# Optimization experiments

Measured on AMD Instinct MI355X. Metric: run time of the kernel, lower is better.

The kernel has to match this reference:

```python
import jax, jax.numpy as jnp
import numpy as np

N = 50000
E = 400000  # bidirectional: second half is reverse of first half
D = 128
T = 3
EPS = 1e-09


def apply_lambda(x, log_dt, log_lambda_real, lambda_imag, one_minus=False):
    # lambda_complex = exp((-exp(log_lambda_real) + 1j*lambda_imag) * dt)
    dt = jnp.exp(log_dt)
    mag = jnp.exp(-jnp.exp(log_lambda_real) * dt)          # |lambda| [D//2]
    mag = jnp.where(one_minus, 1.0 - mag, mag)
    phase = lambda_imag * dt                                # angle (cos/sin are wrap-invariant)
    c, s = jnp.cos(phase), jnp.sin(phase)
    xp = x.reshape(x.shape[:-1] + (-1, 2))                  # [..., D//2, 2]
    xr = (c * xp[..., 0] - s * xp[..., 1]) * mag
    xi = (s * xp[..., 0] + c * xp[..., 1]) * mag
    return jnp.stack((xr, xi), axis=-1).reshape(x.shape)


def setup_inputs() -> dict:
    key = jax.random.key(0)
    kx, ke1, ke2, k1, k2, k3, k4 = jax.random.split(key, 7)
    x = jax.random.normal(kx, (N, D), dtype=jnp.float32)
    a = jax.random.randint(ke1, (E // 2,), 0, N)
    b = jax.random.randint(ke2, (E // 2,), 0, N)
    edge_index = jnp.stack([jnp.concatenate([a, b]), jnp.concatenate([b, a])], axis=0)
    hidden = D + D
    scale1 = 1.0 / np.sqrt(D)
    scale2 = 1.0 / np.sqrt(hidden)
    return {
        "x": x,
        "edge_index": edge_index,
        "log_dt": jnp.asarray(np.log(0.1), dtype=jnp.float32),
        "log_lambda_real": jnp.full((D // 2,), np.log(0.5), dtype=jnp.float32),
        "lambda_imag": jnp.arange(D // 2, dtype=jnp.float32) * np.pi,
        "W1": jax.random.uniform(k1, (D, hidden), jnp.float32, -scale1, scale1),
        "W2": jax.random.uniform(k2, (D, hidden), jnp.float32, -scale1, scale1),
        "Wp": jax.random.uniform(k3, (hidden, D), jnp.float32, -scale2, scale2),
        "bp": jax.random.uniform(k4, (D,), jnp.float32, -scale2, scale2),
    }


def reference(x, edge_index, log_dt, log_lambda_real, lambda_imag, W1, W2, Wp, bp):
    x_in = x  # dim_in == dim_out -> residual from pre-MLP input
    # MLP: silu(x W1) * (x W2) -> proj
    h = jax.nn.silu(x @ W1) * (x @ W2)
    x = h @ Wp + bp

    lam = lambda v, om=False: apply_lambda(v, log_dt, log_lambda_real, lambda_imag, om)
    src, dst = edge_index[0], edge_index[1]

    deg = jax.ops.segment_sum(jnp.ones((E,), x.dtype), src, num_segments=N)  # [N]
    M = x[src]                                                              # [E, D]
    m = jax.ops.segment_sum(M, dst, num_segments=N)                         # [N, D]

    for _ in range(T):
        M_ji = jnp.concatenate((M[E // 2:], M[:E // 2]), axis=0)            # reverse-edge message
        x_e = x[src]
        deg_e = deg[src][:, None]
        M = jnp.where(deg_e == 1,
                      x_e,
                      lam(x_e, True) + lam(m[src] - M_ji) / (deg_e - 1 + EPS))
        m = jax.ops.segment_sum(M, dst, num_segments=N)

    out = jnp.where(deg[:, None] == 0, x, lam(x, True) + lam(m) / (deg[:, None] + EPS))
    out = jax.nn.relu(out)  # dropout p=0 (eval)
    return x_in + out
```

## Files before the change

kernel.cpp:

```cpp
#include <hip/hip_runtime.h>

#define EPSF 1e-9f

typedef __bf16 bf16x8 __attribute__((ext_vector_type(8)));
typedef float  f32x4  __attribute__((ext_vector_type(4)));
typedef unsigned short ushort_t;
typedef unsigned int uint_t;
typedef ushort_t us8 __attribute__((ext_vector_type(8)));

__device__ __forceinline__ float2 cmul(float cr, float ci, float2 v) {
    return make_float2(cr * v.x - ci * v.y, ci * v.x + cr * v.y);
}

__device__ __forceinline__ ushort_t f2bf(float f) {
    unsigned int u = __float_as_uint(f);
    u += 0x7FFFu + ((u >> 16) & 1u);
    return (ushort_t)(u >> 16);
}

__device__ __forceinline__ float2 bfu2(uint_t u) {
    return make_float2(__uint_as_float(u << 16), __uint_as_float(u & 0xFFFF0000u));
}
__device__ __forceinline__ uint_t packbf(float2 v) {
    return ((uint_t)f2bf(v.y) << 16) | (uint_t)f2bf(v.x);
}

__global__ void k_init(const float* __restrict__ ldt, const float* __restrict__ llr,
                       const float* __restrict__ lim, float* __restrict__ tab,
                       int* __restrict__ cnt, int N) {
    int i = blockIdx.x * blockDim.x + threadIdx.x;
    if (i < N) cnt[i] = 0;
    if (blockIdx.x == 0 && threadIdx.x < 64) {
        int p = threadIdx.x;
        float dt  = expf(ldt[0]);
        float mag = expf(-expf(llr[p]) * dt);
        float ph  = lim[p] * dt;
        float c = cosf(ph), s = sinf(ph);
        float m2 = mag * mag, m3 = m2 * mag;
        float c2 = c * c - s * s, s2 = 2.f * c * s;
        float c3 = c2 * c - s2 * s, s3 = s2 * c + c2 * s;
        tab[p]        = c * mag;          tab[64 + p]  = s * mag;
        tab[128 + p]  = c * (1.f - mag);  tab[192 + p] = s * (1.f - mag);
        tab[256 + p]  = c2 * m2;          tab[320 + p] = s2 * m2;
        tab[384 + p]  = c3 * m3;          tab[448 + p] = s3 * m3;
    }
}

__global__ void k_prepw3(const float* __restrict__ W1, const float* __restrict__ W2,
                         const float* __restrict__ Wp, ushort_t* __restrict__ wb1,
                         ushort_t* __restrict__ wb2, ushort_t* __restrict__ wpb) {
    int tid = blockIdx.x * blockDim.x + threadIdx.x;
    const float* w; ushort_t* wb; int ncols, nsteps;
    if (tid < 4096)       { w = W1; wb = wb1; ncols = 256; nsteps = 4; }
    else if (tid < 8192)  { tid -= 4096; w = W2; wb = wb2; ncols = 256; nsteps = 4; }
    else                  { tid -= 8192; w = Wp; wb = wpb; ncols = 128; nsteps = 8; }
    int l  = tid & 63;
    int s  = (tid >> 6) % nsteps;
    int nt = tid / (64 * nsteps);
    int col = nt * 16 + (l & 15);
    int kb  = s * 32 + (l >> 4) * 8;
    us8 d;
#pragma unroll
    for (int j = 0; j < 8; ++j) d[j] = f2bf(w[(size_t)(kb + j) * ncols + col]);
    *(us8*)(wb + (size_t)tid * 8) = d;
}

__global__ void __launch_bounds__(256)
k_mlpf(const float* __restrict__ x, const ushort_t* __restrict__ wb1,
       const ushort_t* __restrict__ wb2, const ushort_t* __restrict__ wpb,
       const float* __restrict__ bp, ushort_t* __restrict__ xpb, int Mt) {
    __shared__ ushort_t hs[2][4096];
    const int wid = threadIdx.x >> 6, l = threadIdx.x & 63;
    const int mt0 = blockIdx.x * 2;
    const bool has1 = (mt0 + 1) < Mt;
    const int llo = l & 15, lhi = l >> 4;

    bf16x8 af[2][4];
#pragma unroll
    for (int m = 0; m < 2; ++m) {
        int mt = (m == 1 && !has1) ? mt0 : (mt0 + m);
        const float* xr = x + (size_t)(mt * 16 + llo) * 128 + lhi * 8;
#pragma unroll
        for (int s = 0; s < 4; ++s) {
            float4 v0 = *(const float4*)(xr + s * 32);
            float4 v1 = *(const float4*)(xr + s * 32 + 4);
            us8 d;
            d[0] = f2bf(v0.x); d[1] = f2bf(v0.y); d[2] = f2bf(v0.z); d[3] = f2bf(v0.w);
            d[4] = f2bf(v1.x); d[5] = f2bf(v1.y); d[6] = f2bf(v1.z); d[7] = f2bf(v1.w);
            af[m][s] = *(bf16x8*)&d;
        }
    }

    const bf16x8* B1 = (const bf16x8*)wb1;
    const bf16x8* B2 = (const bf16x8*)wb2;
    const bf16x8* BP = (const bf16x8*)wpb;
    const f32x4 zero = {0.f, 0.f, 0.f, 0.f};

#pragma unroll
    for (int j = 0; j < 4; ++j) {
        int nt = wid * 4 + j;
        bf16x8 b1[4], b2[4];
#pragma unroll
        for (int s = 0; s < 4; ++s) {
            b1[s] = B1[(nt * 4 + s) * 64 + l];
            b2[s] = B2[(nt * 4 + s) * 64 + l];
        }
#pragma unroll
        for (int m = 0; m < 2; ++m) {
            f32x4 a1 = zero, a2 = zero;
#pragma unroll
            for (int s = 0; s < 4; ++s) {
                a1 = __builtin_amdgcn_mfma_f32_16x16x32_bf16(af[m][s], b1[s], a1, 0, 0, 0);
                a2 = __builtin_amdgcn_mfma_f32_16x16x32_bf16(af[m][s], b2[s], a2, 0, 0, 0);
            }
#pragma unroll
            for (int i = 0; i < 4; ++i) {
                float g = a1[i];
                float hv = (g / (1.f + __expf(-g))) * a2[i];
                int r = 4 * lhi + i;
                int byte = (r << 9) + ((nt * 16 + llo) << 1);
                byte ^= (r & 7) << 4;
                hs[m][byte >> 1] = f2bf(hv);
            }
        }
    }
    __syncthreads();

#pragma unroll
    for (int j = 0; j < 2; ++j) {
        int nt3 = wid * 2 + j;
        f32x4 acc0 = zero, acc1 = zero;
#pragma unroll
        for (int sg = 0; sg < 8; ++sg) {
            bf16x8 bw = BP[(nt3 * 8 + sg) * 64 + l];
            int byte = (llo << 9) + (sg << 6) + (lhi << 4);
            byte ^= (llo & 7) << 4;
            bf16x8 h0 = *(const bf16x8*)((const char*)hs[0] + byte);
            acc0 = __builtin_amdgcn_mfma_f32_16x16x32_bf16(h0, bw, acc0, 0, 0, 0);
            bf16x8 h1 = *(const bf16x8*)((const char*)hs[1] + byte);
            acc1 = __builtin_amdgcn_mfma_f32_16x16x32_bf16(h1, bw, acc1, 0, 0, 0);
        }
        float bpv = bp[nt3 * 16 + llo];
        {
            const int row0 = mt0 * 16;
#pragma unroll
            for (int i = 0; i < 4; ++i) {
                int r = row0 + 4 * lhi + i;
                xpb[(size_t)r * 128 + nt3 * 16 + llo] = f2bf(acc0[i] + bpv);
            }
        }
        if (has1) {
            const int row0 = (mt0 + 1) * 16;
#pragma unroll
            for (int i = 0; i < 4; ++i) {
                int r = row0 + 4 * lhi + i;
                xpb[(size_t)r * 128 + nt3 * 16 + llo] = f2bf(acc1[i] + bpv);
            }
        }
    }
}

__global__ void k_hist(const int* __restrict__ ei, int E, int* __restrict__ cnt) {
    int e = blockIdx.x * blockDim.x + threadIdx.x;
    if (e < E) atomicAdd(&cnt[ei[E + e]], 1);
}

__global__ void __launch_bounds__(256)
k_scanA(const int* __restrict__ cnt, int N, int* __restrict__ bsum) {
    __shared__ int s[256];
    int t = threadIdx.x;
    int i = blockIdx.x * 256 + t;
    int v = (i < N) ? cnt[i] : 0;
    s[t] = v;
    __syncthreads();
#pragma unroll
    for (int d = 128; d > 0; d >>= 1) {
        if (t < d) s[t] += s[t + d];
        __syncthreads();
    }
    if (t == 0) bsum[blockIdx.x] = s[0];
}

__global__ void __launch_bounds__(1024)
k_scanB(const int* __restrict__ bsum, int NB, int* __restrict__ bpre,
        int* __restrict__ offN) {
    __shared__ int s[1024];
    int t = threadIdx.x;
    int v = (t < NB) ? bsum[t] : 0;
    s[t] = v;
    __syncthreads();
    for (int d = 1; d < 1024; d <<= 1) {
        int u = (t >= d) ? s[t - d] : 0;
        __syncthreads();
        s[t] += u;
        __syncthreads();
    }
    if (t < NB) bpre[t] = s[t] - v;
    if (t == NB - 1) *offN = s[t];
}

__global__ void __launch_bounds__(256)
k_scanC(const int* __restrict__ cnt, int N, const int* __restrict__ bpre,
        int* __restrict__ off, int* __restrict__ cursor, float* __restrict__ bv) {
    __shared__ int s[256];
    int t = threadIdx.x;
    int i = blockIdx.x * 256 + t;
    int v = (i < N) ? cnt[i] : 0;
    s[t] = v;
    __syncthreads();
    for (int d = 1; d < 256; d <<= 1) {
        int u = (t >= d) ? s[t - d] : 0;
        __syncthreads();
        s[t] += u;
        __syncthreads();
    }
    if (i < N) {
        int excl = bpre[blockIdx.x] + s[t] - v;
        off[i] = excl;
        cursor[i] = excl;
        bv[i] = (v > 1) ? (-1.f / ((float)v - 1.f + EPSF)) : 0.f;
    }
}

__global__ void k_fill(const int* __restrict__ ei, int E, const float* __restrict__ bv,
                       int* __restrict__ cursor, uint2* __restrict__ csrb) {
    int e = blockIdx.x * blockDim.x + threadIdx.x;
    if (e < E) {
        int s = ei[e], d = ei[E + e];
        int p = atomicAdd(&cursor[d], 1);
        csrb[p] = make_uint2((uint_t)s, __float_as_uint(bv[s]));
    }
}

__global__ void __launch_bounds__(256)
k_passA(const ushort_t* __restrict__ xpb, const uint2* __restrict__ eb,
        const int* __restrict__ off, const float* __restrict__ tab,
        ushort_t* __restrict__ Xbb, ushort_t* __restrict__ a1b, int N) {
    int tid = blockIdx.x * blockDim.x + threadIdx.x;
    int v = tid >> 6, l = tid & 63;
    if (v >= N) return;
    int beg = off[v], end = off[v + 1];
    float2 m0 = make_float2(0.f, 0.f), xb = make_float2(0.f, 0.f);
    const uint_t* tb = (const uint_t*)xpb;
    int k = beg;
    for (; k + 7 < end; k += 8) {
        uint2 e[8];
#pragma unroll
        for (int j = 0; j < 8; ++j) e[j] = eb[k + j];
        uint_t u[8];
#pragma unroll
        for (int j = 0; j < 8; ++j) u[j] = tb[(size_t)e[j].x * 64 + l];
#pragma unroll
        for (int j = 0; j < 8; ++j) {
            float b = __uint_as_float(e[j].y);
            float2 t0 = bfu2(u[j]);
            m0.x += t0.x; m0.y += t0.y;
            xb.x += b * t0.x; xb.y += b * t0.y;
        }
    }
    for (; k < end; ++k) {
        uint2 e0 = eb[k];
        float2 t0 = bfu2(tb[(size_t)e0.x * 64 + l]);
        float b0 = __uint_as_float(e0.y);
        m0.x += t0.x; m0.y += t0.y;
        xb.x += b0 * t0.x; xb.y += b0 * t0.y;
    }
    ((uint_t*)Xbb)[(size_t)v * 64 + l] = packbf(xb);
    float2 xv = bfu2(tb[(size_t)v * 64 + l]);
    int dg = end - beg;
    float L1r = tab[l], L1i = tab[64 + l], O1r = tab[128 + l], O1i = tab[192 + l];
    float Q = 1.f / ((float)dg - 1.f + EPSF);
    float2 t1 = cmul(O1r, O1i, xv);
    float2 t2 = cmul(L1r, L1i, m0);
    float2 a = make_float2(t1.x + Q * t2.x, t1.y + Q * t2.y);
    if (dg == 1) a = xv;
    ((uint_t*)a1b)[(size_t)v * 64 + l] = packbf(a);
}

__global__ void __launch_bounds__(256)
k_passB(const ushort_t* __restrict__ xpb, const ushort_t* __restrict__ a1b,
        const uint2* __restrict__ eb, const int* __restrict__ off,
        const float* __restrict__ tab, ushort_t* __restrict__ ab1b,
        float* __restrict__ Bv, float* __restrict__ B2v,
        ushort_t* __restrict__ a2b, int N) {
    int tid = blockIdx.x * blockDim.x + threadIdx.x;
    int v = tid >> 6, l = tid & 63;
    if (v >= N) return;
    int beg = off[v], end = off[v + 1];
    float2 A1 = make_float2(0.f, 0.f), ab = make_float2(0.f, 0.f);
    float Bs = 0.f, B2s = 0.f;
    const uint_t* tb = (const uint_t*)a1b;
    int k = beg;
    for (; k + 7 < end; k += 8) {
        uint2 e[8];
#pragma unroll
        for (int j = 0; j < 8; ++j) e[j] = eb[k + j];
        uint_t u[8];
#pragma unroll
        for (int j = 0; j < 8; ++j) u[j] = tb[(size_t)e[j].x * 64 + l];
#pragma unroll
        for (int j = 0; j < 8; ++j) {
            float b = __uint_as_float(e[j].y);
            float2 t0 = bfu2(u[j]);
            A1.x += t0.x; A1.y += t0.y;
            ab.x += b * t0.x; ab.y += b * t0.y;
            Bs += b; B2s += b * b;
        }
    }
    for (; k < end; ++k) {
        uint2 e0 = eb[k];
        float2 t0 = bfu2(tb[(size_t)e0.x * 64 + l]);
        float b0 = __uint_as_float(e0.y);
        A1.x += t0.x; A1.y += t0.y;
        ab.x += b0 * t0.x; ab.y += b0 * t0.y;
        Bs += b0; B2s += b0 * b0;
    }
    ((uint_t*)ab1b)[(size_t)v * 64 + l] = packbf(ab);
    if (l == 0) { Bv[v] = Bs; B2v[v] = B2s; }
    float2 xv = bfu2(((const uint_t*)xpb)[(size_t)v * 64 + l]);
    int dg = end - beg;
    float L1r = tab[l], L1i = tab[64 + l], O1r = tab[128 + l], O1i = tab[192 + l];
    float2 lx = cmul(L1r, L1i, xv);
    float2 m1 = make_float2(A1.x + Bs * lx.x, A1.y + Bs * lx.y);
    float Q = 1.f / ((float)dg - 1.f + EPSF);
    float2 t1 = cmul(O1r, O1i, xv);
    float2 lm = cmul(L1r, L1i, m1);
    float2 a = make_float2(t1.x + Q * lm.x, t1.y + Q * lm.y);
    if (dg == 1) a = xv;
    ((uint_t*)a2b)[(size_t)v * 64 + l] = packbf(a);
}

__global__ void __launch_bounds__(256)
k_passC(const ushort_t* __restrict__ xpb, const ushort_t* __restrict__ a2b,
        const ushort_t* __restrict__ a1b, const ushort_t* __restrict__ Xbb,
        const float* __restrict__ bv, const float* __restrict__ Bv,
        const uint2* __restrict__ eb, const int* __restrict__ off,
        const float* __restrict__ tab, ushort_t* __restrict__ a3b, int N) {
    int tid = blockIdx.x * blockDim.x + threadIdx.x;
    int v = tid >> 6, l = tid & 63;
    if (v >= N) return;
    int beg = off[v], end = off[v + 1];
    float2 A2 = make_float2(0.f, 0.f);
    const uint_t* tb = (const uint_t*)a2b;
    int k = beg;
    for (; k + 7 < end; k += 8) {
        uint_t u[8];
#pragma unroll
        for (int j = 0; j < 8; ++j) u[j] = tb[(size_t)eb[k + j].x * 64 + l];
#pragma unroll
        for (int j = 0; j < 8; ++j) {
            float2 t0 = bfu2(u[j]);
            A2.x += t0.x; A2.y += t0.y;
        }
    }
    for (; k < end; ++k) {
        float2 t0 = bfu2(tb[(size_t)eb[k].x * 64 + l]);
        A2.x += t0.x; A2.y += t0.y;
    }
    float2 xv  = bfu2(((const uint_t*)xpb)[(size_t)v * 64 + l]);
    float2 a1v = bfu2(((const uint_t*)a1b)[(size_t)v * 64 + l]);
    float2 Xbv = bfu2(((const uint_t*)Xbb)[(size_t)v * 64 + l]);
    int dg = end - beg;
    float Bs = Bv[v], bs = bv[v];
    float L1r = tab[l], L1i = tab[64 + l], O1r = tab[128 + l], O1i = tab[192 + l];
    float L2r = tab[256 + l], L2i = tab[320 + l];
    float2 la1 = cmul(L1r, L1i, a1v);
    float2 lxb = cmul(L2r, L2i, Xbv);
    float2 m2 = make_float2(A2.x + Bs * la1.x + bs * lxb.x,
                            A2.y + Bs * la1.y + bs * lxb.y);
    float Q = 1.f / ((float)dg - 1.f + EPSF);
    float2 t1 = cmul(O1r, O1i, xv);
    float2 lm = cmul(L1r, L1i, m2);
    float2 a = make_float2(t1.x + Q * lm.x, t1.y + Q * lm.y);
    if (dg == 1) a = xv;
    ((uint_t*)a3b)[(size_t)v * 64 + l] = packbf(a);
}

__global__ void __launch_bounds__(256)
k_passD(const float* __restrict__ xin, const ushort_t* __restrict__ xpb,
        const ushort_t* __restrict__ a3b, const ushort_t* __restrict__ a2b,
        const ushort_t* __restrict__ ab1b, const float* __restrict__ bv,
        const float* __restrict__ Bv, const float* __restrict__ B2v,
        const uint2* __restrict__ eb, const int* __restrict__ off,
        const float* __restrict__ tab, float* __restrict__ out, int N) {
    int tid = blockIdx.x * blockDim.x + threadIdx.x;
    int v = tid >> 6, l = tid & 63;
    if (v >= N) return;
    int beg = off[v], end = off[v + 1];
    float2 A3 = make_float2(0.f, 0.f);
    const uint_t* tb = (const uint_t*)a3b;
    int k = beg;
    for (; k + 7 < end; k += 8) {
        uint_t u[8];
#pragma unroll
        for (int j = 0; j < 8; ++j) u[j] = tb[(size_t)eb[k + j].x * 64 + l];
#pragma unroll
        for (int j = 0; j < 8; ++j) {
            float2 t0 = bfu2(u[j]);
            A3.x += t0.x; A3.y += t0.y;
        }
    }
    for (; k < end; ++k) {
        float2 t0 = bfu2(tb[(size_t)eb[k].x * 64 + l]);
        A3.x += t0.x; A3.y += t0.y;
    }
    size_t o = (size_t)v * 128 + 2 * l;
    float2 xv  = bfu2(((const uint_t*)xpb)[(size_t)v * 64 + l]);
    float2 a2v = bfu2(((const uint_t*)a2b)[(size_t)v * 64 + l]);
    float2 Abv = bfu2(((const uint_t*)ab1b)[(size_t)v * 64 + l]);
    int dg = end - beg;
    float Bs = Bv[v], bs = bv[v], B2s = B2v[v];
    float L1r = tab[l], L1i = tab[64 + l], O1r = tab[128 + l], O1i = tab[192 + l];
    float L2r = tab[256 + l], L2i = tab[320 + l];
    float L3r = tab[384 + l], L3i = tab[448 + l];
    float2 la2 = cmul(L1r, L1i, a2v);
    float2 lab = cmul(L2r, L2i, Abv);
    float2 lx3 = cmul(L3r, L3i, xv);
    float bB2 = bs * B2s;
    float2 m3 = make_float2(A3.x + Bs * la2.x + bs * lab.x + bB2 * lx3.x,
                            A3.y + Bs * la2.y + bs * lab.y + bB2 * lx3.y);
    float2 g;
    if (dg == 0) {
        g = xv;
    } else {
        float inv = 1.f / ((float)dg + EPSF);
        float2 t1 = cmul(O1r, O1i, xv);
        float2 lm = cmul(L1r, L1i, m3);
        g = make_float2(t1.x + lm.x * inv, t1.y + lm.y * inv);
    }
    float2 xi = *(const float2*)&xin[o];
    float2 res = make_float2(xi.x + fmaxf(g.x, 0.f), xi.y + fmaxf(g.y, 0.f));
    *(float2*)&out[o] = res;
}

extern "C" void kernel_launch(void* const* d_in, const int* in_sizes, int n_in,
                              void* d_out, int out_size, void* d_ws, size_t ws_size,
                              hipStream_t stream) {
    const float* x   = (const float*)d_in[0];
    const int*   ei  = (const int*)d_in[1];
    const float* ldt = (const float*)d_in[2];
    const float* llr = (const float*)d_in[3];
    const float* lim = (const float*)d_in[4];
    const float* W1  = (const float*)d_in[5];
    const float* W2  = (const float*)d_in[6];
    const float* Wp  = (const float*)d_in[7];
    const float* bp  = (const float*)d_in[8];
    float* out = (float*)d_out;

    const int N = in_sizes[0] / 128;
    const int E = in_sizes[1] / 2;
    const size_t nd = (size_t)N * 128;
    const int Mt = (N + 15) / 16;
    const int Mt2 = (Mt + 1) / 2;
    const int NB = (N + 255) / 256;

    ushort_t* xpb  = (ushort_t*)d_ws;
    ushort_t* a1b  = xpb + nd;
    ushort_t* a2b  = a1b + nd;
    ushort_t* a3b  = a2b + nd;
    ushort_t* Xbb  = a3b + nd;
    ushort_t* ab1b = Xbb + nd;

    int*   cnt    = (int*)(ab1b + nd);
    int*   off    = cnt + N;
    int*   cursor = off + N + 4;
    float* bv     = (float*)(cursor + N);
    float* Bv     = bv + N;
    float* B2v    = Bv + N;
    float* tab    = B2v + N;
    int*   bsum   = (int*)(tab + 512);
    int*   bpre   = bsum + NB;
    uint2* csrb   = (uint2*)(bpre + NB + (NB & 1));
    ushort_t* wb1 = (ushort_t*)(csrb + E);
    ushort_t* wb2 = wb1 + 32768;
    ushort_t* wpb = wb2 + 32768;

    const int nodeBlocks = (int)(((size_t)N * 64 + 255) / 256);
    const int eBlocks    = (E + 255) / 256;

    k_init<<<NB, 256, 0, stream>>>(ldt, llr, lim, tab, cnt, N);

    k_prepw3<<<48, 256, 0, stream>>>(W1, W2, Wp, wb1, wb2, wpb);
    k_mlpf<<<Mt2, 256, 0, stream>>>(x, wb1, wb2, wpb, bp, xpb, Mt);

    k_hist<<<eBlocks, 256, 0, stream>>>(ei, E, cnt);
    k_scanA<<<NB, 256, 0, stream>>>(cnt, N, bsum);
    k_scanB<<<1, 1024, 0, stream>>>(bsum, NB, bpre, &off[N]);
    k_scanC<<<NB, 256, 0, stream>>>(cnt, N, bpre, off, cursor, bv);
    k_fill<<<eBlocks, 256, 0, stream>>>(ei, E, bv, cursor, csrb);

    k_passA<<<nodeBlocks, 256, 0, stream>>>(xpb, csrb, off, tab, Xbb, a1b, N);
    k_passB<<<nodeBlocks, 256, 0, stream>>>(xpb, a1b, csrb, off, tab, ab1b, Bv, B2v, a2b, N);
    k_passC<<<nodeBlocks, 256, 0, stream>>>(xpb, a2b, a1b, Xbb, bv, Bv, csrb, off, tab, a3b, N);
    k_passD<<<nodeBlocks, 256, 0, stream>>>(x, xpb, a3b, a2b, ab1b, bv, Bv, B2v, csrb, off, tab, out, N);
}
```

Measured before the change: 239.8 us.

## Pad CSR segments to multiples of eight with dummy zero-row edges

Each node's CSR segment is rounded up to a multiple of 8 entries and filled with dummy edges that point to an extra all-zero row at index N, appended to each gathered bf16 buffer. This lets every gather pass run only the unrolled 8-wide loop with no scalar tail, and the true degree now comes from cnt. The cost is an extra kernel that pre-fills the padded edge array, more gather traffic for the padding entries (mean degree is about 8), and extra workspace.

```diff
diff --git a/kernel.cpp b/kernel.cpp
--- a/kernel.cpp
+++ b/kernel.cpp
@@ -27,7 +27,9 @@
 
 __global__ void k_init(const float* __restrict__ ldt, const float* __restrict__ llr,
                        const float* __restrict__ lim, float* __restrict__ tab,
-                       int* __restrict__ cnt, int N) {
+                       int* __restrict__ cnt, int N,
+                       uint_t* __restrict__ xpbu, uint_t* __restrict__ a1bu,
+                       uint_t* __restrict__ a2bu, uint_t* __restrict__ a3bu) {
     int i = blockIdx.x * blockDim.x + threadIdx.x;
     if (i < N) cnt[i] = 0;
     if (blockIdx.x == 0 && threadIdx.x < 64) {
@@ -44,6 +46,10 @@
         tab[256 + p]  = c2 * m2;          tab[320 + p] = s2 * m2;
         tab[384 + p]  = c3 * m3;          tab[448 + p] = s3 * m3;
     }
+    if (blockIdx.x == 1 && threadIdx.x < 64) {
+        size_t o = (size_t)N * 64 + threadIdx.x;
+        xpbu[o] = 0u; a1bu[o] = 0u; a2bu[o] = 0u; a3bu[o] = 0u;
+    }
 }
 
 __global__ void k_prepw3(const float* __restrict__ W1, const float* __restrict__ W2,
@@ -170,7 +176,7 @@
     __shared__ int s[256];
     int t = threadIdx.x;
     int i = blockIdx.x * 256 + t;
-    int v = (i < N) ? cnt[i] : 0;
+    int v = (i < N) ? ((cnt[i] + 7) & ~7) : 0;
     s[t] = v;
     __syncthreads();
 #pragma unroll
@@ -205,7 +211,8 @@
     __shared__ int s[256];
     int t = threadIdx.x;
     int i = blockIdx.x * 256 + t;
-    int v = (i < N) ? cnt[i] : 0;
+    int c = (i < N) ? cnt[i] : 0;
+    int v = (c + 7) & ~7;
     s[t] = v;
     __syncthreads();
     for (int d = 1; d < 256; d <<= 1) {
@@ -218,8 +225,13 @@
         int excl = bpre[blockIdx.x] + s[t] - v;
         off[i] = excl;
         cursor[i] = excl;
-        bv[i] = (v > 1) ? (-1.f / ((float)v - 1.f + EPSF)) : 0.f;
-    }
+        bv[i] = (c > 1) ? (-1.f / ((float)c - 1.f + EPSF)) : 0.f;
+    }
+}
+
+__global__ void k_predummy(uint2* __restrict__ csrb, int total, int N) {
+    int i = blockIdx.x * blockDim.x + threadIdx.x;
+    if (i < total) csrb[i] = make_uint2((uint_t)N, 0u);
 }
 
 __global__ void k_fill(const int* __restrict__ ei, int E, const float* __restrict__ bv,
@@ -234,7 +246,8 @@
 
 __global__ void __launch_bounds__(256)
 k_passA(const ushort_t* __restrict__ xpb, const uint2* __restrict__ eb,
-        const int* __restrict__ off, const float* __restrict__ tab,
+        const int* __restrict__ off, const int* __restrict__ cnt,
+        const float* __restrict__ tab,
         ushort_t* __restrict__ Xbb, ushort_t* __restrict__ a1b, int N) {
     int tid = blockIdx.x * blockDim.x + threadIdx.x;
     int v = tid >> 6, l = tid & 63;
@@ -242,8 +255,7 @@
     int beg = off[v], end = off[v + 1];
     float2 m0 = make_float2(0.f, 0.f), xb = make_float2(0.f, 0.f);
     const uint_t* tb = (const uint_t*)xpb;
-    int k = beg;
-    for (; k + 7 < end; k += 8) {
+    for (int k = beg; k < end; k += 8) {
         uint2 e[8];
 #pragma unroll
         for (int j = 0; j < 8; ++j) e[j] = eb[k + j];
@@ -258,16 +270,9 @@
             xb.x += b * t0.x; xb.y += b * t0.y;
         }
     }
-    for (; k < end; ++k) {
-        uint2 e0 = eb[k];
-        float2 t0 = bfu2(tb[(size_t)e0.x * 64 + l]);
-        float b0 = __uint_as_float(e0.y);
-        m0.x += t0.x; m0.y += t0.y;
-        xb.x += b0 * t0.x; xb.y += b0 * t0.y;
-    }
     ((uint_t*)Xbb)[(size_t)v * 64 + l] = packbf(xb);
     float2 xv = bfu2(tb[(size_t)v * 64 + l]);
-    int dg = end - beg;
+    int dg = cnt[v];
     float L1r = tab[l], L1i = tab[64 + l], O1r = tab[128 + l], O1i = tab[192 + l];
     float Q = 1.f / ((float)dg - 1.f + EPSF);
     float2 t1 = cmul(O1r, O1i, xv);
@@ -280,8 +285,8 @@
 __global__ void __launch_bounds__(256)
 k_passB(const ushort_t* __restrict__ xpb, const ushort_t* __restrict__ a1b,
         const uint2* __restrict__ eb, const int* __restrict__ off,
-        const float* __restrict__ tab, ushort_t* __restrict__ ab1b,
-        float* __restrict__ Bv, float* __restrict__ B2v,
+        const int* __restrict__ cnt, const float* __restrict__ tab,
+        ushort_t* __restrict__ ab1b, float* __restrict__ Bv, float* __restrict__ B2v,
         ushort_t* __restrict__ a2b, int N) {
     int tid = blockIdx.x * blockDim.x + threadIdx.x;
     int v = tid >> 6, l = tid & 63;
@@ -290,8 +295,7 @@
     float2 A1 = make_float2(0.f, 0.f), ab = make_float2(0.f, 0.f);
     float Bs = 0.f, B2s = 0.f;
     const uint_t* tb = (const uint_t*)a1b;
-    int k = beg;
-    for (; k + 7 < end; k += 8) {
+    for (int k = beg; k < end; k += 8) {
         uint2 e[8];
 #pragma unroll
         for (int j = 0; j < 8; ++j) e[j] = eb[k + j];
@@ -307,18 +311,10 @@
             Bs += b; B2s += b * b;
         }
     }
-    for (; k < end; ++k) {
-        uint2 e0 = eb[k];
-        float2 t0 = bfu2(tb[(size_t)e0.x * 64 + l]);
-        float b0 = __uint_as_float(e0.y);
-        A1.x += t0.x; A1.y += t0.y;
-        ab.x += b0 * t0.x; ab.y += b0 * t0.y;
-        Bs += b0; B2s += b0 * b0;
-    }
     ((uint_t*)ab1b)[(size_t)v * 64 + l] = packbf(ab);
     if (l == 0) { Bv[v] = Bs; B2v[v] = B2s; }
     float2 xv = bfu2(((const uint_t*)xpb)[(size_t)v * 64 + l]);
-    int dg = end - beg;
+    int dg = cnt[v];
     float L1r = tab[l], L1i = tab[64 + l], O1r = tab[128 + l], O1i = tab[192 + l];
     float2 lx = cmul(L1r, L1i, xv);
     float2 m1 = make_float2(A1.x + Bs * lx.x, A1.y + Bs * lx.y);
@@ -335,15 +331,15 @@
         const ushort_t* __restrict__ a1b, const ushort_t* __restrict__ Xbb,
         const float* __restrict__ bv, const float* __restrict__ Bv,
         const uint2* __restrict__ eb, const int* __restrict__ off,
-        const float* __restrict__ tab, ushort_t* __restrict__ a3b, int N) {
+        const int* __restrict__ cnt, const float* __restrict__ tab,
+        ushort_t* __restrict__ a3b, int N) {
     int tid = blockIdx.x * blockDim.x + threadIdx.x;
     int v = tid >> 6, l = tid & 63;
     if (v >= N) return;
     int beg = off[v], end = off[v + 1];
     float2 A2 = make_float2(0.f, 0.f);
     const uint_t* tb = (const uint_t*)a2b;
-    int k = beg;
-    for (; k + 7 < end; k += 8) {
+    for (int k = beg; k < end; k += 8) {
         uint_t u[8];
 #pragma unroll
         for (int j = 0; j < 8; ++j) u[j] = tb[(size_t)eb[k + j].x * 64 + l];
@@ -353,14 +349,10 @@
             A2.x += t0.x; A2.y += t0.y;
         }
     }
-    for (; k < end; ++k) {
-        float2 t0 = bfu2(tb[(size_t)eb[k].x * 64 + l]);
-        A2.x += t0.x; A2.y += t0.y;
-    }
     float2 xv  = bfu2(((const uint_t*)xpb)[(size_t)v * 64 + l]);
     float2 a1v = bfu2(((const uint_t*)a1b)[(size_t)v * 64 + l]);
     float2 Xbv = bfu2(((const uint_t*)Xbb)[(size_t)v * 64 + l]);
-    int dg = end - beg;
+    int dg = cnt[v];
     float Bs = Bv[v], bs = bv[v];
     float L1r = tab[l], L1i = tab[64 + l], O1r = tab[128 + l], O1i = tab[192 + l];
     float L2r = tab[256 + l], L2i = tab[320 + l];
@@ -382,15 +374,15 @@
         const ushort_t* __restrict__ ab1b, const float* __restrict__ bv,
         const float* __restrict__ Bv, const float* __restrict__ B2v,
         const uint2* __restrict__ eb, const int* __restrict__ off,
-        const float* __restrict__ tab, float* __restrict__ out, int N) {
+        const int* __restrict__ cnt, const float* __restrict__ tab,
+        float* __restrict__ out, int N) {
     int tid = blockIdx.x * blockDim.x + threadIdx.x;
     int v = tid >> 6, l = tid & 63;
     if (v >= N) return;
     int beg = off[v], end = off[v + 1];
     float2 A3 = make_float2(0.f, 0.f);
     const uint_t* tb = (const uint_t*)a3b;
-    int k = beg;
-    for (; k + 7 < end; k += 8) {
+    for (int k = beg; k < end; k += 8) {
         uint_t u[8];
 #pragma unroll
         for (int j = 0; j < 8; ++j) u[j] = tb[(size_t)eb[k + j].x * 64 + l];
@@ -399,16 +391,12 @@
             float2 t0 = bfu2(u[j]);
             A3.x += t0.x; A3.y += t0.y;
         }
-    }
-    for (; k < end; ++k) {
-        float2 t0 = bfu2(tb[(size_t)eb[k].x * 64 + l]);
-        A3.x += t0.x; A3.y += t0.y;
     }
     size_t o = (size_t)v * 128 + 2 * l;
     float2 xv  = bfu2(((const uint_t*)xpb)[(size_t)v * 64 + l]);
     float2 a2v = bfu2(((const uint_t*)a2b)[(size_t)v * 64 + l]);
     float2 Abv = bfu2(((const uint_t*)ab1b)[(size_t)v * 64 + l]);
-    int dg = end - beg;
+    int dg = cnt[v];
     float Bs = Bv[v], bs = bv[v], B2s = B2v[v];
     float L1r = tab[l], L1i = tab[64 + l], O1r = tab[128 + l], O1i = tab[192 + l];
     float L2r = tab[256 + l], L2i = tab[320 + l];
@@ -449,16 +437,18 @@
 
     const int N = in_sizes[0] / 128;
     const int E = in_sizes[1] / 2;
-    const size_t nd = (size_t)N * 128;
+    const size_t nd  = (size_t)N * 128;
+    const size_t nd2 = nd + 128;
     const int Mt = (N + 15) / 16;
     const int Mt2 = (Mt + 1) / 2;
     const int NB = (N + 255) / 256;
+    const int EPAD = E + 7 * N;
 
     ushort_t* xpb  = (ushort_t*)d_ws;
-    ushort_t* a1b  = xpb + nd;
-    ushort_t* a2b  = a1b + nd;
-    ushort_t* a3b  = a2b + nd;
-    ushort_t* Xbb  = a3b + nd;
+    ushort_t* a1b  = xpb + nd2;
+    ushort_t* a2b  = a1b + nd2;
+    ushort_t* a3b  = a2b + nd2;
+    ushort_t* Xbb  = a3b + nd2;
     ushort_t* ab1b = Xbb + nd;
 
     int*   cnt    = (int*)(ab1b + nd);
@@ -471,14 +461,15 @@
     int*   bsum   = (int*)(tab + 512);
     int*   bpre   = bsum + NB;
     uint2* csrb   = (uint2*)(bpre + NB + (NB & 1));
-    ushort_t* wb1 = (ushort_t*)(csrb + E);
+    ushort_t* wb1 = (ushort_t*)(csrb + EPAD);
     ushort_t* wb2 = wb1 + 32768;
     ushort_t* wpb = wb2 + 32768;
 
     const int nodeBlocks = (int)(((size_t)N * 64 + 255) / 256);
     const int eBlocks    = (E + 255) / 256;
 
-    k_init<<<NB, 256, 0, stream>>>(ldt, llr, lim, tab, cnt, N);
+    k_init<<<NB, 256, 0, stream>>>(ldt, llr, lim, tab, cnt, N,
+                                   (uint_t*)xpb, (uint_t*)a1b, (uint_t*)a2b, (uint_t*)a3b);
 
     k_prepw3<<<48, 256, 0, stream>>>(W1, W2, Wp, wb1, wb2, wpb);
     k_mlpf<<<Mt2, 256, 0, stream>>>(x, wb1, wb2, wpb, bp, xpb, Mt);
@@ -487,10 +478,11 @@
     k_scanA<<<NB, 256, 0, stream>>>(cnt, N, bsum);
     k_scanB<<<1, 1024, 0, stream>>>(bsum, NB, bpre, &off[N]);
     k_scanC<<<NB, 256, 0, stream>>>(cnt, N, bpre, off, cursor, bv);
+    k_predummy<<<(EPAD + 255) / 256, 256, 0, stream>>>(csrb, EPAD, N);
     k_fill<<<eBlocks, 256, 0, stream>>>(ei, E, bv, cursor, csrb);
 
-    k_passA<<<nodeBlocks, 256, 0, stream>>>(xpb, csrb, off, tab, Xbb, a1b, N);
-    k_passB<<<nodeBlocks, 256, 0, stream>>>(xpb, a1b, csrb, off, tab, ab1b, Bv, B2v, a2b, N);
-    k_passC<<<nodeBlocks, 256, 0, stream>>>(xpb, a2b, a1b, Xbb, bv, Bv, csrb, off, tab, a3b, N);
-    k_passD<<<nodeBlocks, 256, 0, stream>>>(x, xpb, a3b, a2b, ab1b, bv, Bv, B2v, csrb, off, tab, out, N);
-}
+    k_passA<<<nodeBlocks, 256, 0, stream>>>(xpb, csrb, off, cnt, tab, Xbb, a1b, N);
+    k_passB<<<nodeBlocks, 256, 0, stream>>>(xpb, a1b, csrb, off, cnt, tab, ab1b, Bv, B2v, a2b, N);
+    k_passC<<<nodeBlocks, 256, 0, stream>>>(xpb, a2b, a1b, Xbb, bv, Bv, csrb, off, cnt, tab, a3b, N);
+    k_passD<<<nodeBlocks, 256, 0, stream>>>(x, xpb, a3b, a2b, ab1b, bv, Bv, B2v, csrb, off, cnt, tab, out, N);
+}
```

Result: faster. 224.3 us (-6.5%).
